# Optimization experiments

Hardware: AMD Instinct MI355X
Metric: run time of the kernel (lower is better)

Reference implementation:

```python
import jax, jax.numpy as jnp
import numpy as np
from jax import lax

MU = 0.1          # cfg MODEL.MU (FISTA step size)
LMBD = 0.1        # cfg MODEL.LAMBDA[0]
N_STEPS = 4       # cfg MODEL.NUM_LAYERS (unrolled FISTA iterations)
BN_EPS = 1e-5


def _norm_w(W):
    # DictBlock w_norm: each dictionary filter normalized to unit L2 norm.
    # torch does this under no_grad (in-place on .data), so the norm is a constant.
    n = jnp.sqrt(jnp.sum(W * W, axis=(1, 2, 3), keepdims=True))
    return W / lax.stop_gradient(n + 1e-12)


def _conv(x, W, stride, pad):
    return lax.conv_general_dilated(x, W, (stride, stride), [(pad, pad)] * 2,
                                    dimension_numbers=('NCHW', 'OIHW', 'NCHW'))


def _conv_t(z, W, stride, pad, out_pad):
    # torch conv_transpose2d(z, W, stride, padding=pad, output_padding=out_pad)
    k = W.shape[2]
    Wt = jnp.transpose(jnp.flip(W, (2, 3)), (1, 0, 2, 3))  # (in_ch, dict, k, k)
    p = k - 1 - pad
    return lax.conv_general_dilated(z, Wt, (1, 1), [(p, p + out_pad)] * 2,
                                    lhs_dilation=(stride, stride),
                                    dimension_numbers=('NCHW', 'OIHW', 'NCHW'))


def _shrink(c):
    # non-negative soft threshold: relu(c - lmbd*step)
    return jax.nn.relu(c - LMBD * MU)


def _dict_conv(x, W, stride):
    # Unrolled FISTA sparse coding: min_c 0.5||x - W^T c||^2 + lmbd||c||_1, c>=0
    W = _norm_w(W)
    out_pad = stride - 1
    c = _shrink(MU * _conv(x, W, stride, 1))
    c_pre = jnp.zeros_like(c)
    t = 1.0
    for _ in range(N_STEPS - 1):
        t_next = (1.0 + float(np.sqrt(1.0 + 4.0 * t * t))) / 2.0
        a = c + ((t - 1.0) / t_next) * (c - c_pre)
        c_pre = c
        r = x - _conv_t(a, W, stride, 1, out_pad)       # reconstruction residual
        c = _shrink(a + MU * _conv(r, W, stride, 1))    # proximal gradient step
        t = t_next
    return c


def _bn(x, g, b, m, v):
    # eval-mode BatchNorm2d with running stats
    scale = g * lax.rsqrt(v + BN_EPS)
    return (x - m[None, :, None, None]) * scale[None, :, None, None] + b[None, :, None, None]


def setup_inputs() -> dict:
    key = jax.random.key(0)
    ks = jax.random.split(key, 12)
    N, Cin, Cout, H = 32, 128, 256, 56
    x = jax.random.normal(ks[0], (N, Cin, H, H), jnp.float32)
    def unit_norm(W):
        return W / (jnp.sqrt(jnp.sum(W * W, axis=(1, 2, 3), keepdims=True)) + 1e-12)
    W1 = unit_norm(jax.random.normal(ks[1], (Cout, Cin, 3, 3), jnp.float32))
    W2 = unit_norm(jax.random.normal(ks[2], (Cout, Cout, 3, 3), jnp.float32))
    Wsc = jax.random.normal(ks[3], (Cout, Cin, 1, 1), jnp.float32) * 0.05
    def bn(k):
        k1, k2, k3, k4 = jax.random.split(k, 4)
        g = 1.0 + 0.1 * jax.random.normal(k1, (Cout,), jnp.float32)
        b = 0.1 * jax.random.normal(k2, (Cout,), jnp.float32)
        m = 0.1 * jax.random.normal(k3, (Cout,), jnp.float32)
        v = 0.5 + jax.random.uniform(k4, (Cout,), jnp.float32)
        return g, b, m, v
    bn1_g, bn1_b, bn1_m, bn1_v = bn(ks[4])
    bn2_g, bn2_b, bn2_m, bn2_v = bn(ks[5])
    bnsc_g, bnsc_b, bnsc_m, bnsc_v = bn(ks[6])
    return dict(x=x, W1=W1, W2=W2, Wsc=Wsc,
                bn1_g=bn1_g, bn1_b=bn1_b, bn1_m=bn1_m, bn1_v=bn1_v,
                bn2_g=bn2_g, bn2_b=bn2_b, bn2_m=bn2_m, bn2_v=bn2_v,
                bnsc_g=bnsc_g, bnsc_b=bnsc_b, bnsc_m=bnsc_m, bnsc_v=bnsc_v)


def reference(x, W1, W2, Wsc,
              bn1_g, bn1_b, bn1_m, bn1_v,
              bn2_g, bn2_b, bn2_m, bn2_v,
              bnsc_g, bnsc_b, bnsc_m, bnsc_v):
    out = _bn(_dict_conv(x, W1, 2), bn1_g, bn1_b, bn1_m, bn1_v)
    out = _bn(_dict_conv(out, W2, 1), bn2_g, bn2_b, bn2_m, bn2_v)
    sc = _bn(_conv(x, Wsc, 2, 0), bnsc_g, bnsc_b, bnsc_m, bnsc_v)
    return jax.nn.relu(out + sc)
```

## Files before the change

kernel.cpp:

```cpp
#include <hip/hip_runtime.h>
#include <math.h>

#define MU_F 0.1f
#define SHRINK_F 0.01f
#define BN_EPS_F 1e-5f

typedef _Float16 half_t;
typedef _Float16 half8 __attribute__((ext_vector_type(8)));
typedef float f32x4 __attribute__((ext_vector_type(4)));

__device__ __forceinline__ void gll16(const half_t* g, half_t* l) {
    __builtin_amdgcn_global_load_lds(
        (const __attribute__((address_space(1))) void*)g,
        (__attribute__((address_space(3))) void*)l, 16, 0, 0);
}

#define VM_WAIT_BARRIER(N) do {                                   \
    asm volatile("s_waitcnt vmcnt(" #N ")" ::: "memory");         \
    __builtin_amdgcn_s_barrier();                                 \
    __builtin_amdgcn_sched_barrier(0);                            \
} while (0)

template<int KS, int S, int PAD, int MODE>
__global__ __launch_bounds__(128, 2)
void conv_big(const half_t* __restrict__ Ag, const half_t* __restrict__ Xh,
              float* __restrict__ outF, half_t* __restrict__ outH,
              const half_t* __restrict__ auxH, const float* __restrict__ auxF,
              int CA, int Cout, int Hin, int Win, int Hout, int Wout, int ptiles,
              float alpha, float beta, float delta, int relu1,
              const float* __restrict__ pscale, const float* __restrict__ pbias,
              const float* __restrict__ aux3, int relu2,
              const half_t* __restrict__ zpg)
{
    __shared__ __align__(16) half_t sm[3 * 6144];

    const int tid = threadIdx.x;
    const int wv = tid >> 6, ln = tid & 63;
    const int co0 = blockIdx.y * 128;
    const int wco = wv * 64;

    int bx = blockIdx.x;
    {
        const int cpx = gridDim.x >> 3;
        bx = (bx & 7) * cpx + (bx >> 3);
    }

    int eh = 0, ew = 0, p0;
    if (MODE == 2) {
        int q = bx / ptiles;
        p0 = (bx - q * ptiles) * 64;
        eh = q >> 1; ew = q & 1;
    } else {
        p0 = bx * 64;
    }

    const int Wd   = (MODE == 2) ? (Wout >> 1) : Wout;
    const int Hd   = (MODE == 2) ? (Hout >> 1) : Hout;
    const int PHW1 = Hd * Wd;
    const int NPX  = PHW1 * 32;
    const int K9   = KS * KS * CA;

    const int r  = tid >> 2;
    const int s4 = tid & 3;
    const int sw = (s4 ^ (r & 3)) << 3;

    const size_t abase0 = (size_t)(co0 + r     ) * K9;
    const size_t abase1 = (size_t)(co0 + r + 32) * K9;
    const size_t abase2 = (size_t)(co0 + r + 64) * K9;
    const size_t abase3 = (size_t)(co0 + r + 96) * K9;

    int bph[2], bpw[2]; bool bval[2]; size_t bnb[2];
#pragma unroll
    for (int i = 0; i < 2; ++i) {
        int px = p0 + i * 32 + r;
        bval[i] = px < NPX;
        int pc = bval[i] ? px : 0;
        int n2 = pc / PHW1; int rem = pc - n2 * PHW1;
        int ph = rem / Wd;
        bph[i] = ph; bpw[i] = rem - ph * Wd;
        bnb[i] = (size_t)n2 * Hin * Win;
    }

    const int cpt = CA >> 5;
    const int lgc = (cpt == 8) ? 3 : 2;
    int ntap, lgj = 0, phh = 0, pww = 0;
    if (MODE == 2) {
        phh = (eh + 1) & 1; pww = (ew + 1) & 1;
        lgj = ew;
        ntap = (1 + eh) * (1 + ew);
    } else {
        ntap = KS * KS;
    }
    const int total = ntap << lgc;

    auto issue = [&](int flat, half_t* dst) {
        const int ci = flat & (cpt - 1);
        const int ti = flat >> lgc;
        int kh, kw;
        if (MODE == 2) {
            int i2 = ti >> lgj, j = ti & ((1 << lgj) - 1);
            kh = phh + 2 * i2; kw = pww + 2 * j;
        } else if (KS == 3) {
            kh = (ti * 11) >> 5; kw = ti - 3 * kh;
        } else { kh = 0; kw = 0; }
        const int c0 = ci << 5;
        const size_t koff = (size_t)(kh * KS + kw) * CA + c0 + sw;
        gll16(Ag + abase0 + koff, dst +        tid * 8);
        gll16(Ag + abase1 + koff, dst + 1024 + tid * 8);
        gll16(Ag + abase2 + koff, dst + 2048 + tid * 8);
        gll16(Ag + abase3 + koff, dst + 3072 + tid * 8);
#pragma unroll
        for (int i = 0; i < 2; ++i) {
            int hh, ww2; bool ok = bval[i];
            if (MODE == 0) {
                hh = bph[i] * S - PAD + kh; ww2 = bpw[i] * S - PAD + kw;
                ok = ok && (unsigned)hh < (unsigned)Hin && (unsigned)ww2 < (unsigned)Win;
            } else if (MODE == 1) {
                hh = bph[i] + PAD - kh; ww2 = bpw[i] + PAD - kw;
                ok = ok && (unsigned)hh < (unsigned)Hin && (unsigned)ww2 < (unsigned)Win;
            } else {
                int nh = 2 * bph[i] + eh + PAD - kh, nw = 2 * bpw[i] + ew + PAD - kw;
                hh = nh >> 1; ww2 = nw >> 1;
                ok = ok && nh >= 0 && nw >= 0 && hh < Hin && ww2 < Win;
            }
            const half_t* src = ok
                ? Xh + (bnb[i] + (size_t)(hh * Win + ww2)) * CA + c0 + sw
                : zpg;
            gll16(src, dst + 4096 + i * 1024 + tid * 8);
        }
    };

    f32x4 acc[4][4] = {};

    issue(0, sm);
    issue(1, sm + 6144);
    VM_WAIT_BARRIER(6);

    const int fr = ln & 15, q8 = ln >> 4;
    const int rdA = (wco + fr) * 32 + ((q8 ^ (fr & 3)) << 3);
    const int rdB = (128 + fr) * 32 + ((q8 ^ (fr & 3)) << 3);

    int bi = 0;
    for (int k = 0; k < total; ++k) {
        half_t* bufr = sm + bi * 6144;
        if (k + 2 < total) {
            int b2 = bi + 2; if (b2 >= 3) b2 -= 3;
            issue(k + 2, sm + b2 * 6144);
        }
        half8 fa[4], fb[4];
#pragma unroll
        for (int m = 0; m < 4; ++m)
            fa[m] = *(const half8*)(bufr + rdA + m * 512);
#pragma unroll
        for (int t2 = 0; t2 < 4; ++t2)
            fb[t2] = *(const half8*)(bufr + rdB + t2 * 512);
#pragma unroll
        for (int m = 0; m < 4; ++m)
#pragma unroll
            for (int t2 = 0; t2 < 4; ++t2)
                acc[m][t2] = __builtin_amdgcn_mfma_f32_16x16x32_f16(fa[m], fb[t2], acc[m][t2], 0, 0, 0);
        if (k + 2 < total) {
            VM_WAIT_BARRIER(6);
        } else if (k + 1 < total) {
            VM_WAIT_BARRIER(0);
        }
        bi = (bi == 2) ? 0 : bi + 1;
    }

    const int rg = ln >> 4;
#pragma unroll
    for (int t = 0; t < 4; ++t) {
        int px = p0 + t * 16 + fr;
        if (px >= NPX) continue;
        int n2 = px / PHW1; int rem = px - n2 * PHW1;
        int ph = rem / Wd, pw = rem - ph * Wd;
        int oh, ow;
        if (MODE == 2) { oh = 2 * ph + eh; ow = 2 * pw + ew; }
        else           { oh = ph;          ow = pw; }
        size_t ghwc = ((size_t)(n2 * Hout + oh) * Wout + ow) * Cout;
#pragma unroll
        for (int m = 0; m < 4; ++m) {
#pragma unroll
            for (int rr = 0; rr < 4; ++rr) {
                int co_l = co0 + wco + m * 16 + rg * 4 + rr;
                size_t fidx = ((size_t)(n2 * Cout + co_l) * Hout + oh) * Wout + ow;
                float v = alpha * acc[m][t][rr] + delta;
                if (auxH) v += beta * (float)auxH[ghwc + co_l];
                if (auxF) v += beta * auxF[fidx];
                if (relu1) v = fmaxf(v, 0.f);
                if (pscale) v = pscale[co_l] * v + pbias[co_l];
                if (aux3) v += aux3[fidx];
                if (relu2) v = fmaxf(v, 0.f);
                if (outH) outH[ghwc + co_l] = (half_t)v;
                else      outF[fidx] = v;
            }
        }
    }
}

template<int KT>
__global__ __launch_bounds__(256)
void pack_w(const float* __restrict__ W, half_t* __restrict__ Wh,
            half_t* __restrict__ WTh, int Cin, int Cout, int do_norm)
{
    __shared__ float red[256];
    int co = blockIdx.x, tid = threadIdx.x;
    int CK = Cin * KT;
    const float* w = W + (size_t)co * CK;
    float inv = 1.f;
    if (do_norm) {
        float s = 0.f;
        for (int i = tid; i < CK; i += 256) { float v = w[i]; s += v * v; }
        red[tid] = s; __syncthreads();
        for (int o = 128; o > 0; o >>= 1) {
            if (tid < o) red[tid] += red[tid + o];
            __syncthreads();
        }
        inv = 1.f / (sqrtf(red[0]) + 1e-12f);
    }
    for (int i = tid; i < CK; i += 256) {
        int ci = i / KT, tap = i - ci * KT;
        half_t h = (half_t)(w[i] * inv);
        Wh[((size_t)co * KT + tap) * Cin + ci] = h;
        if (WTh) WTh[((size_t)ci * KT + tap) * Cout + co] = h;
    }
}

__global__ __launch_bounds__(256)
void tx_kernel(const float* __restrict__ x, half_t* __restrict__ xTh)
{
    __shared__ __align__(16) half_t tl[56 * 136];
    int h = blockIdx.x, n = blockIdx.y, tid = threadIdx.x;
    for (int it = 0; it < 28; ++it) {
        int id = tid + it * 256;
        int c = id / 56, w0 = id - c * 56;
        tl[w0 * 136 + c] = (half_t)x[(((size_t)n * 128 + c) * 56 + h) * 56 + w0];
    }
    __syncthreads();
    if (tid < 224) {
        int w0 = tid >> 2, part = tid & 3;
        size_t base = (((size_t)n * 56 + h) * 56 + w0) * 128 + part * 32;
#pragma unroll
        for (int j = 0; j < 4; ++j)
            *(half8*)(xTh + base + j * 8) = *(const half8*)(tl + w0 * 136 + part * 32 + j * 8);
    }
}

__global__ __launch_bounds__(256)
void comb_kernel(const half_t* __restrict__ c, const half_t* __restrict__ p,
                 half_t* __restrict__ a, float w1, float w2, int n8)
{
    int i = blockIdx.x * 256 + threadIdx.x;
    if (i >= n8) return;
    half8 cv = ((const half8*)c)[i];
    half8 pv = ((const half8*)p)[i];
    half8 rres;
#pragma unroll
    for (int j = 0; j < 8; ++j) rres[j] = (half_t)(w1 * (float)cv[j] + w2 * (float)pv[j]);
    ((half8*)a)[i] = rres;
}

__global__ __launch_bounds__(256)
void bn_prep_kernel(const float* __restrict__ g, const float* __restrict__ b,
                    const float* __restrict__ m, const float* __restrict__ v,
                    float* __restrict__ s, float* __restrict__ t, int C)
{
    int i = blockIdx.x * 256 + threadIdx.x;
    if (i < C) {
        float sc = g[i] * rsqrtf(v[i] + BN_EPS_F);
        s[i] = sc; t[i] = b[i] - m[i] * sc;
    }
}

__global__ __launch_bounds__(128)
void zfill_kernel(half_t* __restrict__ p)
{
    p[threadIdx.x] = (half_t)0.f;
}

extern "C" void kernel_launch(void* const* d_in, const int* in_sizes, int n_in,
                              void* d_out, int out_size, void* d_ws, size_t ws_size,
                              hipStream_t stream)
{
    (void)in_sizes; (void)n_in; (void)out_size;
    const float* x    = (const float*)d_in[0];
    const float* W1   = (const float*)d_in[1];
    const float* W2   = (const float*)d_in[2];
    const float* Wsc  = (const float*)d_in[3];
    const float* bn1g = (const float*)d_in[4];
    const float* bn1b = (const float*)d_in[5];
    const float* bn1m = (const float*)d_in[6];
    const float* bn1v = (const float*)d_in[7];
    const float* bn2g = (const float*)d_in[8];
    const float* bn2b = (const float*)d_in[9];
    const float* bn2m = (const float*)d_in[10];
    const float* bn2v = (const float*)d_in[11];
    const float* bscg = (const float*)d_in[12];
    const float* bscb = (const float*)d_in[13];
    const float* bscm = (const float*)d_in[14];
    const float* bscv = (const float*)d_in[15];

    const size_t NB = (size_t)32 * 256 * 28 * 28;
    const size_t NX = (size_t)32 * 128 * 56 * 56;

    char* base = (char*)d_ws;
    size_t off = 0;
    auto alloc = [&](size_t nbytes) -> void* {
        void* r = base + off;
        off = (off + nbytes + 255) & ~(size_t)255;
        return r;
    };
    half_t* Wh1  = (half_t*)alloc(294912 * 2);
    half_t* WTh1 = (half_t*)alloc(294912 * 2);
    half_t* Wh2  = (half_t*)alloc(589824 * 2);
    half_t* WTh2 = (half_t*)alloc(589824 * 2);
    half_t* Wsch = (half_t*)alloc(32768 * 2);
    float* bn1s = (float*)alloc(256 * 4);  float* bn1t = (float*)alloc(256 * 4);
    float* bn2s = (float*)alloc(256 * 4);  float* bn2t = (float*)alloc(256 * 4);
    float* bscs = (float*)alloc(256 * 4);  float* bsct = (float*)alloc(256 * 4);
    half_t* zpg  = (half_t*)alloc(256);
    half_t* xTh  = (half_t*)alloc(NX * 2);
    half_t* r56h = xTh;
    half_t* Pa   = (half_t*)alloc(NB * 2);
    half_t* Pb   = (half_t*)alloc(NB * 2);
    half_t* Pc   = (half_t*)alloc(NB * 2);
    half_t* Py   = (half_t*)alloc(NB * 2);
    half_t* r28h = (half_t*)alloc(NB * 2);
    float*  scF  = (float*)alloc(NB * 4);
    if (off > ws_size) return;

    float* outp = (float*)d_out;

    double t = 1.0; float al[3];
    for (int i = 0; i < 3; ++i) {
        double tn = (1.0 + sqrt(1.0 + 4.0 * t * t)) / 2.0;
        al[i] = (float)((t - 1.0) / tn); t = tn;
    }

    const dim3 blk(256);
    const dim3 cblk(128);
    const dim3 gB(392, 2, 1);
    const dim3 gT2(1568, 1, 1);
    const int n8 = (int)(NB / 8);
    const dim3 gC((n8 + 255) / 256);
    const float* NF = nullptr;
    const half_t* NH = nullptr;
    float* NFo = nullptr;
    half_t* NHo = nullptr;

    pack_w<9><<<256, blk, 0, stream>>>(W1, Wh1, WTh1, 128, 256, 1);
    pack_w<9><<<256, blk, 0, stream>>>(W2, Wh2, WTh2, 256, 256, 1);
    pack_w<1><<<256, blk, 0, stream>>>(Wsc, Wsch, nullptr, 128, 256, 0);
    bn_prep_kernel<<<1, blk, 0, stream>>>(bn1g, bn1b, bn1m, bn1v, bn1s, bn1t, 256);
    bn_prep_kernel<<<1, blk, 0, stream>>>(bn2g, bn2b, bn2m, bn2v, bn2s, bn2t, 256);
    bn_prep_kernel<<<1, blk, 0, stream>>>(bscg, bscb, bscm, bscv, bscs, bsct, 256);
    zfill_kernel<<<1, cblk, 0, stream>>>(zpg);
    tx_kernel<<<dim3(56, 32), blk, 0, stream>>>(x, xTh);

    conv_big<3,2,1,0><<<gB, cblk, 0, stream>>>(Wh1, xTh, NFo, Pa, NH, NF,
        128, 256, 56, 56, 28, 28, 392, MU_F, 0.f, -SHRINK_F, 1, NF, NF, NF, 0, zpg);
    conv_big<1,2,0,0><<<gB, cblk, 0, stream>>>(Wsch, xTh, scF, NHo, NH, NF,
        128, 256, 56, 56, 28, 28, 392, 1.f, 0.f, 0.f, 0, bscs, bsct, NF, 0, zpg);

    conv_big<3,2,1,2><<<gT2, cblk, 0, stream>>>(WTh1, Pa, NFo, r56h, NH, x,
        256, 128, 28, 28, 56, 56, 392, -1.f, 1.f, 0.f, 0, NF, NF, NF, 0, zpg);
    conv_big<3,2,1,0><<<gB, cblk, 0, stream>>>(Wh1, r56h, NFo, Pb, Pa, NF,
        128, 256, 56, 56, 28, 28, 392, MU_F, 1.f, -SHRINK_F, 1, NF, NF, NF, 0, zpg);

    comb_kernel<<<gC, blk, 0, stream>>>(Pb, Pa, Pc, 1.f + al[1], -al[1], n8);
    conv_big<3,2,1,2><<<gT2, cblk, 0, stream>>>(WTh1, Pc, NFo, r56h, NH, x,
        256, 128, 28, 28, 56, 56, 392, -1.f, 1.f, 0.f, 0, NF, NF, NF, 0, zpg);
    conv_big<3,2,1,0><<<gB, cblk, 0, stream>>>(Wh1, r56h, NFo, Pa, Pc, NF,
        128, 256, 56, 56, 28, 28, 392, MU_F, 1.f, -SHRINK_F, 1, NF, NF, NF, 0, zpg);

    comb_kernel<<<gC, blk, 0, stream>>>(Pa, Pb, Pc, 1.f + al[2], -al[2], n8);
    conv_big<3,2,1,2><<<gT2, cblk, 0, stream>>>(WTh1, Pc, NFo, r56h, NH, x,
        256, 128, 28, 28, 56, 56, 392, -1.f, 1.f, 0.f, 0, NF, NF, NF, 0, zpg);
    conv_big<3,2,1,0><<<gB, cblk, 0, stream>>>(Wh1, r56h, NFo, Py, Pc, NF,
        128, 256, 56, 56, 28, 28, 392, MU_F, 1.f, -SHRINK_F, 1, bn1s, bn1t, NF, 0, zpg);

    conv_big<3,1,1,0><<<gB, cblk, 0, stream>>>(Wh2, Py, NFo, Pa, NH, NF,
        256, 256, 28, 28, 28, 28, 392, MU_F, 0.f, -SHRINK_F, 1, NF, NF, NF, 0, zpg);

    conv_big<3,1,1,1><<<gB, cblk, 0, stream>>>(WTh2, Pa, NFo, r28h, Py, NF,
        256, 256, 28, 28, 28, 28, 392, -1.f, 1.f, 0.f, 0, NF, NF, NF, 0, zpg);
    conv_big<3,1,1,0><<<gB, cblk, 0, stream>>>(Wh2, r28h, NFo, Pb, Pa, NF,
        256, 256, 28, 28, 28, 28, 392, MU_F, 1.f, -SHRINK_F, 1, NF, NF, NF, 0, zpg);

    comb_kernel<<<gC, blk, 0, stream>>>(Pb, Pa, Pc, 1.f + al[1], -al[1], n8);
    conv_big<3,1,1,1><<<gB, cblk, 0, stream>>>(WTh2, Pc, NFo, r28h, Py, NF,
        256, 256, 28, 28, 28, 28, 392, -1.f, 1.f, 0.f, 0, NF, NF, NF, 0, zpg);
    conv_big<3,1,1,0><<<gB, cblk, 0, stream>>>(Wh2, r28h, NFo, Pa, Pc, NF,
        256, 256, 28, 28, 28, 28, 392, MU_F, 1.f, -SHRINK_F, 1, NF, NF, NF, 0, zpg);

    comb_kernel<<<gC, blk, 0, stream>>>(Pa, Pb, Pc, 1.f + al[2], -al[2], n8);
    conv_big<3,1,1,1><<<gT2.x ? gB : gB, cblk, 0, stream>>>(WTh2, Pc, NFo, r28h, Py, NF,
        256, 256, 28, 28, 28, 28, 392, -1.f, 1.f, 0.f, 0, NF, NF, NF, 0, zpg);
    conv_big<3,1,1,0><<<gB, cblk, 0, stream>>>(Wh2, r28h, outp, NHo, Pc, NF,
        256, 256, 28, 28, 28, 28, 392, MU_F, 1.f, -SHRINK_F, 1, bn2s, bn2t, scF, 1, zpg);
}
```

Baseline: 1.294 ms.

## Enlarge conv tiles to 128x128 with 4 waves and 4-stage LDS pipeline

Makes the implicit-GEMM conv block 256 threads (4 waves in a 2x2 layout) covering 128 output channels by 128 pixels instead of 128x64, halving the grid. This raises operand reuse per LDS tile and cuts redundant weight loads. The LDS ring grows from triple to quadruple buffering (64 KB), with three stages prefetched ahead. The XCD-aware block remapping is generalized to grids not divisible by 8. The larger LDS footprint and fewer blocks (392 for most convs) may reduce occupancy and leave CUs idle on the last wave.

```diff
diff --git a/kernel.cpp b/kernel.cpp
--- a/kernel.cpp
+++ b/kernel.cpp
@@ -22,7 +22,7 @@
 } while (0)
 
 template<int KS, int S, int PAD, int MODE>
-__global__ __launch_bounds__(128, 2)
+__global__ __launch_bounds__(256, 2)
 void conv_big(const half_t* __restrict__ Ag, const half_t* __restrict__ Xh,
               float* __restrict__ outF, half_t* __restrict__ outH,
               const half_t* __restrict__ auxH, const float* __restrict__ auxF,
@@ -32,26 +32,28 @@
               const float* __restrict__ aux3, int relu2,
               const half_t* __restrict__ zpg)
 {
-    __shared__ __align__(16) half_t sm[3 * 6144];
+    __shared__ __align__(16) half_t sm[4 * 8192];
 
     const int tid = threadIdx.x;
     const int wv = tid >> 6, ln = tid & 63;
     const int co0 = blockIdx.y * 128;
-    const int wco = wv * 64;
-
-    int bx = blockIdx.x;
+    const int wco = (wv & 1) * 64, wpx = (wv >> 1) * 64;
+
+    int bx;
     {
-        const int cpx = gridDim.x >> 3;
-        bx = (bx & 7) * cpx + (bx >> 3);
+        const int nwg = gridDim.x;
+        const int q = nwg >> 3, r8 = nwg & 7;
+        const int xcd = blockIdx.x & 7, idx = blockIdx.x >> 3;
+        bx = (xcd < r8 ? xcd * (q + 1) : r8 * (q + 1) + (xcd - r8) * q) + idx;
     }
 
     int eh = 0, ew = 0, p0;
     if (MODE == 2) {
-        int q = bx / ptiles;
-        p0 = (bx - q * ptiles) * 64;
-        eh = q >> 1; ew = q & 1;
+        int qq = bx / ptiles;
+        p0 = (bx - qq * ptiles) * 128;
+        eh = qq >> 1; ew = qq & 1;
     } else {
-        p0 = bx * 64;
+        p0 = bx * 128;
     }
 
     const int Wd   = (MODE == 2) ? (Wout >> 1) : Wout;
@@ -65,14 +67,12 @@
     const int sw = (s4 ^ (r & 3)) << 3;
 
     const size_t abase0 = (size_t)(co0 + r     ) * K9;
-    const size_t abase1 = (size_t)(co0 + r + 32) * K9;
-    const size_t abase2 = (size_t)(co0 + r + 64) * K9;
-    const size_t abase3 = (size_t)(co0 + r + 96) * K9;
+    const size_t abase1 = (size_t)(co0 + r + 64) * K9;
 
     int bph[2], bpw[2]; bool bval[2]; size_t bnb[2];
 #pragma unroll
     for (int i = 0; i < 2; ++i) {
-        int px = p0 + i * 32 + r;
+        int px = p0 + i * 64 + r;
         bval[i] = px < NPX;
         int pc = bval[i] ? px : 0;
         int n2 = pc / PHW1; int rem = pc - n2 * PHW1;
@@ -106,9 +106,7 @@
         const int c0 = ci << 5;
         const size_t koff = (size_t)(kh * KS + kw) * CA + c0 + sw;
         gll16(Ag + abase0 + koff, dst +        tid * 8);
-        gll16(Ag + abase1 + koff, dst + 1024 + tid * 8);
-        gll16(Ag + abase2 + koff, dst + 2048 + tid * 8);
-        gll16(Ag + abase3 + koff, dst + 3072 + tid * 8);
+        gll16(Ag + abase1 + koff, dst + 2048 + tid * 8);
 #pragma unroll
         for (int i = 0; i < 2; ++i) {
             int hh, ww2; bool ok = bval[i];
@@ -126,27 +124,26 @@
             const half_t* src = ok
                 ? Xh + (bnb[i] + (size_t)(hh * Win + ww2)) * CA + c0 + sw
                 : zpg;
-            gll16(src, dst + 4096 + i * 1024 + tid * 8);
+            gll16(src, dst + 4096 + i * 2048 + tid * 8);
         }
     };
 
     f32x4 acc[4][4] = {};
 
     issue(0, sm);
-    issue(1, sm + 6144);
-    VM_WAIT_BARRIER(6);
+    issue(1, sm + 8192);
+    issue(2, sm + 16384);
+    VM_WAIT_BARRIER(8);
 
     const int fr = ln & 15, q8 = ln >> 4;
-    const int rdA = (wco + fr) * 32 + ((q8 ^ (fr & 3)) << 3);
-    const int rdB = (128 + fr) * 32 + ((q8 ^ (fr & 3)) << 3);
-
-    int bi = 0;
+    const int sx = (q8 ^ (fr & 3)) << 3;
+    const int rdA = (wco + fr) * 32 + sx;
+    const int rdB = (128 + wpx + fr) * 32 + sx;
+
     for (int k = 0; k < total; ++k) {
-        half_t* bufr = sm + bi * 6144;
-        if (k + 2 < total) {
-            int b2 = bi + 2; if (b2 >= 3) b2 -= 3;
-            issue(k + 2, sm + b2 * 6144);
-        }
+        half_t* bufr = sm + (k & 3) * 8192;
+        if (k + 3 < total)
+            issue(k + 3, sm + ((k + 3) & 3) * 8192);
         half8 fa[4], fb[4];
 #pragma unroll
         for (int m = 0; m < 4; ++m)
@@ -159,18 +156,15 @@
 #pragma unroll
             for (int t2 = 0; t2 < 4; ++t2)
                 acc[m][t2] = __builtin_amdgcn_mfma_f32_16x16x32_f16(fa[m], fb[t2], acc[m][t2], 0, 0, 0);
-        if (k + 2 < total) {
-            VM_WAIT_BARRIER(6);
-        } else if (k + 1 < total) {
-            VM_WAIT_BARRIER(0);
-        }
-        bi = (bi == 2) ? 0 : bi + 1;
+        if (k + 3 < total)      VM_WAIT_BARRIER(8);
+        else if (k + 2 < total) VM_WAIT_BARRIER(4);
+        else if (k + 1 < total) VM_WAIT_BARRIER(0);
     }
 
     const int rg = ln >> 4;
 #pragma unroll
     for (int t = 0; t < 4; ++t) {
-        int px = p0 + t * 16 + fr;
+        int px = p0 + wpx + t * 16 + fr;
         if (px >= NPX) continue;
         int n2 = px / PHW1; int rem = px - n2 * PHW1;
         int ph = rem / Wd, pw = rem - ph * Wd;
@@ -338,9 +332,9 @@
     }
 
     const dim3 blk(256);
-    const dim3 cblk(128);
-    const dim3 gB(392, 2, 1);
-    const dim3 gT2(1568, 1, 1);
+    const dim3 cblk(256);
+    const dim3 gB(196, 2, 1);
+    const dim3 gT2(784, 1, 1);
     const int n8 = (int)(NB / 8);
     const dim3 gC((n8 + 255) / 256);
     const float* NF = nullptr;
@@ -354,48 +348,48 @@
     bn_prep_kernel<<<1, blk, 0, stream>>>(bn1g, bn1b, bn1m, bn1v, bn1s, bn1t, 256);
     bn_prep_kernel<<<1, blk, 0, stream>>>(bn2g, bn2b, bn2m, bn2v, bn2s, bn2t, 256);
     bn_prep_kernel<<<1, blk, 0, stream>>>(bscg, bscb, bscm, bscv, bscs, bsct, 256);
-    zfill_kernel<<<1, cblk, 0, stream>>>(zpg);
+    zfill_kernel<<<1, dim3(128), 0, stream>>>(zpg);
     tx_kernel<<<dim3(56, 32), blk, 0, stream>>>(x, xTh);
 
     conv_big<3,2,1,0><<<gB, cblk, 0, stream>>>(Wh1, xTh, NFo, Pa, NH, NF,
-        128, 256, 56, 56, 28, 28, 392, MU_F, 0.f, -SHRINK_F, 1, NF, NF, NF, 0, zpg);
+        128, 256, 56, 56, 28, 28, 196, MU_F, 0.f, -SHRINK_F, 1, NF, NF, NF, 0, zpg);
     conv_big<1,2,0,0><<<gB, cblk, 0, stream>>>(Wsch, xTh, scF, NHo, NH, NF,
-        128, 256, 56, 56, 28, 28, 392, 1.f, 0.f, 0.f, 0, bscs, bsct, NF, 0, zpg);
+        128, 256, 56, 56, 28, 28, 196, 1.f, 0.f, 0.f, 0, bscs, bsct, NF, 0, zpg);
 
     conv_big<3,2,1,2><<<gT2, cblk, 0, stream>>>(WTh1, Pa, NFo, r56h, NH, x,
-        256, 128, 28, 28, 56, 56, 392, -1.f, 1.f, 0.f, 0, NF, NF, NF, 0, zpg);
+        256, 128, 28, 28, 56, 56, 196, -1.f, 1.f, 0.f, 0, NF, NF, NF, 0, zpg);
     conv_big<3,2,1,0><<<gB, cblk, 0, stream>>>(Wh1, r56h, NFo, Pb, Pa, NF,
-        128, 256, 56, 56, 28, 28, 392, MU_F, 1.f, -SHRINK_F, 1, NF, NF, NF, 0, zpg);
+        128, 256, 56, 56, 28, 28, 196, MU_F, 1.f, -SHRINK_F, 1, NF, NF, NF, 0, zpg);
 
     comb_kernel<<<gC, blk, 0, stream>>>(Pb, Pa, Pc, 1.f + al[1], -al[1], n8);
     conv_big<3,2,1,2><<<gT2, cblk, 0, stream>>>(WTh1, Pc, NFo, r56h, NH, x,
-        256, 128, 28, 28, 56, 56, 392, -1.f, 1.f, 0.f, 0, NF, NF, NF, 0, zpg);
+        256, 128, 28, 28, 56, 56, 196, -1.f, 1.f, 0.f, 0, NF, NF, NF, 0, zpg);
     conv_big<3,2,1,0><<<gB, cblk, 0, stream>>>(Wh1, r56h, NFo, Pa, Pc, NF,
-        128, 256, 56, 56, 28, 28, 392, MU_F, 1.f, -SHRINK_F, 1, NF, NF, NF, 0, zpg);
+        128, 256, 56, 56, 28, 28, 196, MU_F, 1.f, -SHRINK_F, 1, NF, NF, NF, 0, zpg);
 
     comb_kernel<<<gC, blk, 0, stream>>>(Pa, Pb, Pc, 1.f + al[2], -al[2], n8);
     conv_big<3,2,1,2><<<gT2, cblk, 0, stream>>>(WTh1, Pc, NFo, r56h, NH, x,
-        256, 128, 28, 28, 56, 56, 392, -1.f, 1.f, 0.f, 0, NF, NF, NF, 0, zpg);
+        256, 128, 28, 28, 56, 56, 196, -1.f, 1.f, 0.f, 0, NF, NF, NF, 0, zpg);
     conv_big<3,2,1,0><<<gB, cblk, 0, stream>>>(Wh1, r56h, NFo, Py, Pc, NF,
-        128, 256, 56, 56, 28, 28, 392, MU_F, 1.f, -SHRINK_F, 1, bn1s, bn1t, NF, 0, zpg);
+        128, 256, 56, 56, 28, 28, 196, MU_F, 1.f, -SHRINK_F, 1, bn1s, bn1t, NF, 0, zpg);
 
     conv_big<3,1,1,0><<<gB, cblk, 0, stream>>>(Wh2, Py, NFo, Pa, NH, NF,
-        256, 256, 28, 28, 28, 28, 392, MU_F, 0.f, -SHRINK_F, 1, NF, NF, NF, 0, zpg);
+        256, 256, 28, 28, 28, 28, 196, MU_F, 0.f, -SHRINK_F, 1, NF, NF, NF, 0, zpg);
 
     conv_big<3,1,1,1><<<gB, cblk, 0, stream>>>(WTh2, Pa, NFo, r28h, Py, NF,
-        256, 256, 28, 28, 28, 28, 392, -1.f, 1.f, 0.f, 0, NF, NF, NF, 0, zpg);
+        256, 256, 28, 28, 28, 28, 196, -1.f, 1.f, 0.f, 0, NF, NF, NF, 0, zpg);
     conv_big<3,1,1,0><<<gB, cblk, 0, stream>>>(Wh2, r28h, NFo, Pb, Pa, NF,
-        256, 256, 28, 28, 28, 28, 392, MU_F, 1.f, -SHRINK_F, 1, NF, NF, NF, 0, zpg);
+        256, 256, 28, 28, 28, 28, 196, MU_F, 1.f, -SHRINK_F, 1, NF, NF, NF, 0, zpg);
 
     comb_kernel<<<gC, blk, 0, stream>>>(Pb, Pa, Pc, 1.f + al[1], -al[1], n8);
     conv_big<3,1,1,1><<<gB, cblk, 0, stream>>>(WTh2, Pc, NFo, r28h, Py, NF,
-        256, 256, 28, 28, 28, 28, 392, -1.f, 1.f, 0.f, 0, NF, NF, NF, 0, zpg);
+        256, 256, 28, 28, 28, 28, 196, -1.f, 1.f, 0.f, 0, NF, NF, NF, 0, zpg);
     conv_big<3,1,1,0><<<gB, cblk, 0, stream>>>(Wh2, r28h, NFo, Pa, Pc, NF,
-        256, 256, 28, 28, 28, 28, 392, MU_F, 1.f, -SHRINK_F, 1, NF, NF, NF, 0, zpg);
+        256, 256, 28, 28, 28, 28, 196, MU_F, 1.f, -SHRINK_F, 1, NF, NF, NF, 0, zpg);
 
     comb_kernel<<<gC, blk, 0, stream>>>(Pa, Pb, Pc, 1.f + al[2], -al[2], n8);
-    conv_big<3,1,1,1><<<gT2.x ? gB : gB, cblk, 0, stream>>>(WTh2, Pc, NFo, r28h, Py, NF,
-        256, 256, 28, 28, 28, 28, 392, -1.f, 1.f, 0.f, 0, NF, NF, NF, 0, zpg);
+    conv_big<3,1,1,1><<<gB, cblk, 0, stream>>>(WTh2, Pc, NFo, r28h, Py, NF,
+        256, 256, 28, 28, 28, 28, 196, -1.f, 1.f, 0.f, 0, NF, NF, NF, 0, zpg);
     conv_big<3,1,1,0><<<gB, cblk, 0, stream>>>(Wh2, r28h, outp, NHo, Pc, NF,
-        256, 256, 28, 28, 28, 28, 392, MU_F, 1.f, -SHRINK_F, 1, bn2s, bn2t, scF, 1, zpg);
-}
+        256, 256, 28, 28, 28, 28, 196, MU_F, 1.f, -SHRINK_F, 1, bn2s, bn2t, scF, 1, zpg);
+}
```

New measurement: 1.236 ms. 1.05x faster.
